# Kernel tuning notes

Measured on AMD Instinct MI355X. Metric: run time of the kernel, lower is better.

## Reference

```python
import jax, jax.numpy as jnp
import numpy as np
from jax import lax
from math import sqrt

STYLE_DIM = 512
K = 3


def _equal_linear(latent, w, b):
    # EqualLinear: runtime weight scaling by 1/sqrt(fan_in)
    scale = 1.0 / sqrt(latent.shape[1])
    return latent @ (w.T * scale) + b


def _pixel_norm(x, axis=1, eps=1e-8):
    return x * jax.lax.rsqrt(jnp.mean(x * x, axis=axis, keepdims=True) + eps)


def _modconv(x, latent, weight, bias, el_w, el_b):
    # weight: (nc2, nc1, 3, 3); x: (B, nc1, H, W); latent: (B, style_dim)
    b = x.shape[0]
    nc2, nc1, k, _ = weight.shape
    fan_in = nc1 * k * k
    w = weight * sqrt(2.0 / fan_in)                      # (nc2, nc1, 3, 3)
    # style: s = 1 + PixelNorm(EqualLinear(latent))      # (B, nc1)
    s = 1.0 + _pixel_norm(_equal_linear(latent, el_w, el_b), axis=1)
    # demod: d_bo = rsqrt(sum_{c,k} (s_bc * w_ock)^2 + 1e-5)
    wsq = jnp.sum(w * w, axis=(2, 3))                    # (nc2, nc1)
    d = jax.lax.rsqrt(jnp.einsum('bc,oc->bo', s * s, wsq) + 1e-5)  # (B, nc2)
    # conv(x, s*w)*d  ==  conv(s*x, w)*d  (s is per input channel)
    xm = x * s[:, :, None, None]
    y = lax.conv_general_dilated(
        xm, w, window_strides=(1, 1), padding=[(1, 1), (1, 1)],
        dimension_numbers=('NCHW', 'OIHW', 'NCHW'))
    return y * d[:, :, None, None] + bias


def _style_block(x, latent, w0, b0, el0_w, el0_b, w1, b1, el1_w, el1_b):
    act_gain = sqrt(2.0)
    out = _modconv(x, latent, w0, b0, el0_w, el0_b)
    out = jax.nn.leaky_relu(out, 0.2) * act_gain
    out = _pixel_norm(out, axis=1)
    out = _modconv(out, latent, w1, b1, el1_w, el1_b)
    out = jax.nn.leaky_relu(out, 0.2) * act_gain
    out = _pixel_norm(out, axis=1)
    return out


def setup_inputs() -> dict:
    key = jax.random.key(0)
    ks = jax.random.split(key, 8)
    B, NC1, NC2, H, W = 8, 256, 256, 128, 128
    return {
        'x': jax.random.normal(ks[0], (B, NC1, H, W), jnp.float32),
        'latent': jax.random.normal(ks[1], (B, STYLE_DIM), jnp.float32),
        'w0': jax.random.normal(ks[2], (NC2, NC1, K, K), jnp.float32),
        'b0': jnp.zeros((1, NC2, 1, 1), jnp.float32),
        'el0_w': jax.random.normal(ks[3], (NC1, STYLE_DIM), jnp.float32),
        'el0_b': jnp.zeros((NC1,), jnp.float32),
        'w1': jax.random.normal(ks[4], (NC2, NC2, K, K), jnp.float32),
        'b1': jnp.zeros((1, NC2, 1, 1), jnp.float32),
        'el1_w': jax.random.normal(ks[5], (NC2, STYLE_DIM), jnp.float32),
        'el1_b': jnp.zeros((NC2,), jnp.float32),
    }


def reference(x, latent, w0, b0, el0_w, el0_b, w1, b1, el1_w, el1_b):
    return _style_block(x, latent, w0, b0, el0_w, el0_b, w1, b1, el1_w, el1_b)
```

## Files before the change

kernel.cpp:

```cpp
#include <hip/hip_runtime.h>
#include <hip/hip_bf16.h>

typedef __attribute__((ext_vector_type(8))) short short8;
typedef __attribute__((ext_vector_type(16))) float f32x16;

typedef const __attribute__((address_space(1))) unsigned int* gas1_t;
typedef __attribute__((address_space(3))) unsigned int* las3_t;

__device__ __forceinline__ unsigned short f2bf(float x) {
    unsigned int u = __float_as_uint(x);
    u = (u + 0x7fffu + ((u >> 16) & 1u)) >> 16;
    return (unsigned short)u;
}

__device__ __forceinline__ int4 pack8(const unsigned short* u) {
    int4 p;
    p.x = (int)((unsigned)u[0] | ((unsigned)u[1] << 16));
    p.y = (int)((unsigned)u[2] | ((unsigned)u[3] << 16));
    p.z = (int)((unsigned)u[4] | ((unsigned)u[5] << 16));
    p.w = (int)((unsigned)u[6] | ((unsigned)u[7] << 16));
    return p;
}

__device__ __forceinline__ void gld_lds16(const void* g, void* l) {
    __builtin_amdgcn_global_load_lds((gas1_t)g, (las3_t)l, 16, 0, 0);
}

__global__ void style_kernel(const float* __restrict__ latent,
                             const float* __restrict__ elw0, const float* __restrict__ elb0,
                             const float* __restrict__ elw1, const float* __restrict__ elb1,
                             float* __restrict__ s_arr) {
    const int cv = blockIdx.x >> 3;
    const int b  = blockIdx.x & 7;
    const int c  = threadIdx.x;
    const float* elw = cv ? elw1 : elw0;
    const float* elb = cv ? elb1 : elb0;

    __shared__ float lat[512];
    lat[c] = latent[b * 512 + c];
    lat[c + 256] = latent[b * 512 + c + 256];
    __syncthreads();

    float accv = 0.f;
    const float* wrow = elw + (size_t)c * 512;
#pragma unroll 8
    for (int k = 0; k < 512; ++k) accv += lat[k] * wrow[k];
    const float lin = accv * 0.04419417382415922f + elb[c];

    float sq = lin * lin;
#pragma unroll
    for (int off = 32; off >= 1; off >>= 1) sq += __shfl_xor(sq, off);
    __shared__ float wsum[4];
    if ((threadIdx.x & 63) == 0) wsum[threadIdx.x >> 6] = sq;
    __syncthreads();
    const float total = wsum[0] + wsum[1] + wsum[2] + wsum[3];
    const float s = 1.0f + lin * rsqrtf(total * (1.0f / 256.0f) + 1e-8f);
    s_arr[(cv * 8 + b) * 256 + c] = s;
}

__global__ void wsq_kernel(const float* __restrict__ w0, const float* __restrict__ w1,
                           float* __restrict__ wsq) {
    const int cv = blockIdx.x >> 8;
    const int o  = blockIdx.x & 255;
    const int c  = threadIdx.x;
    const float* w = cv ? w1 : w0;
    const size_t base = ((size_t)o * 256 + c) * 9;
    float ssum = 0.f;
#pragma unroll
    for (int t = 0; t < 9; ++t) { float v = w[base + t]; ssum += v * v; }
    wsq[((size_t)cv * 256 + o) * 256 + c] = ssum * (2.0f / 2304.0f);
}

__global__ void demod_kernel(const float* __restrict__ s_arr, const float* __restrict__ wsq,
                             float* __restrict__ d_arr) {
    const int cv = blockIdx.x >> 3;
    const int b  = blockIdx.x & 7;
    const int o  = threadIdx.x;
    __shared__ float ss[256];
    float sv = s_arr[(cv * 8 + b) * 256 + o];
    ss[o] = sv * sv;
    __syncthreads();
    const float* wrow = wsq + ((size_t)cv * 256 + o) * 256;
    float accv = 0.f;
#pragma unroll 8
    for (int c = 0; c < 256; ++c) accv += ss[c] * wrow[c];
    d_arr[(cv * 8 + b) * 256 + o] = rsqrtf(accv + 1e-5f);
}

__global__ void fold_kernel(const float* __restrict__ w0, const float* __restrict__ w1,
                            const float* __restrict__ s_arr, const float* __restrict__ d_arr,
                            unsigned short* __restrict__ wm0, unsigned short* __restrict__ wm1) {
    const int cv = blockIdx.y;
    const int e  = blockIdx.x * 256 + threadIdx.x;
    const float* w = cv ? w1 : w0;
    unsigned short* wm = cv ? wm1 : wm0;
    const int slab = e >> 13;
    const int idx  = e & 8191;
    const int b  = slab / 72;
    const int s2 = slab - b * 72;
    const int cc = s2 / 9;
    const int t  = s2 - cc * 9;
    const int o  = idx >> 5;
    const int c5 = idx & 31;
    const int c  = cc * 32 + c5;
    const float val = w[((size_t)o * 256 + c) * 9 + t] * 0.029462782549439483f
                    * s_arr[(cv * 8 + b) * 256 + c] * d_arr[(cv * 8 + b) * 256 + o];
    wm[((size_t)slab << 13) + (c5 >> 3) * 2048 + o * 8 + (c5 & 7)] = f2bf(val);
}

__global__ void convert_kernel(const float* __restrict__ x, unsigned short* __restrict__ xq) {
    const int blk = blockIdx.x;
    const int hh  = blk & 127;
    const int bg_ = blk >> 7;
    const int g   = bg_ & 31;
    const int b   = bg_ >> 5;
    __shared__ float sx[8][128];
    const int tid = threadIdx.x;
#pragma unroll
    for (int i = 0; i < 4; ++i) {
        const int idx = tid + i * 256;
        const int c8 = idx >> 7, p = idx & 127;
        sx[c8][p] = x[(((size_t)b * 256 + g * 8 + c8) * 128 + hh) * 128 + p];
    }
    __syncthreads();
    if (tid < 128) {
        const int p = tid;
        unsigned short u[8];
#pragma unroll
        for (int j = 0; j < 8; ++j) u[j] = f2bf(sx[j][p]);
        *(int4*)(xq + ((((size_t)b * 32 + g) * 128 + hh) * 128 + p) * 8) = pack8(u);
    }
}

template<bool FINAL_OUT>
__global__ __launch_bounds__(512, 2) void conv_kernel(
    const unsigned short* __restrict__ in_q, const unsigned short* __restrict__ wmod,
    const float* __restrict__ bias, const unsigned short* __restrict__ zpg,
    void* __restrict__ out_v) {

    __shared__ __align__(16) char lds[87104];

    const int tid  = threadIdx.x;
    const int b    = blockIdx.x & 7;
    const int rp   = blockIdx.x >> 3;
    const int h0   = rp * 2;
    const int lane = tid & 63;
    const int wr   = tid >> 6;
    const int wm   = wr & 3;
    const int wn   = wr >> 2;
    const int l31  = lane & 31;
    const int khg  = lane >> 5;

    float* sbias = (float*)(lds + 81984);
    if (tid < 256) sbias[tid] = bias[tid];
    if (tid < 4)   *(int4*)(lds + 81920 + tid * 16) = (int4){0, 0, 0, 0};

    int aoff[2][2];
#pragma unroll
    for (int mb = 0; mb < 2; ++mb)
#pragma unroll
        for (int kh = 0; kh < 2; ++kh)
            aoff[mb][kh] = ((khg + 2 * kh) * 256 + wm * 64 + mb * 32 + l31) * 16;

    const unsigned short* wmb = wmod + (size_t)b * 589824;
    const unsigned short* xqb = in_q + (size_t)b * 4194304;

    auto issueA = [&](const char* src, int buf) {
        char* db = lds + buf * 16384 + wr * 2048;
        const char* s = src + wr * 2048 + lane * 16;
        gld_lds16(s,        db);
        gld_lds16(s + 1024, db + 1024);
    };

    auto issueB = [&](int cc) {
        const int chunk = tid >> 7, px = tid & 127;
#pragma unroll
        for (int r = 0; r < 4; ++r) {
            const int hin = h0 - 1 + r;
            const unsigned short* src = ((unsigned)hin < 128u)
                ? xqb + (((size_t)(cc * 4 + chunk) * 128 + hin) * 128 + px) * 8
                : zpg;
            gld_lds16(src, lds + 49152 + r * 8192 + wr * 1024);
        }
    };

    f32x16 acc[2][4];
#pragma unroll
    for (int mb = 0; mb < 2; ++mb)
#pragma unroll
        for (int nb = 0; nb < 4; ++nb)
#pragma unroll
            for (int r = 0; r < 16; ++r) acc[mb][nb][r] = 0.f;

    issueB(0);
    issueA((const char*)wmb, 0);
    issueA((const char*)wmb + 16384, 1);
    __syncthreads();

    const char* gA = (const char*)wmb + 32768;
#pragma unroll 1
    for (int cc = 0; cc < 8; ++cc) {
#pragma unroll
        for (int t = 0; t < 9; ++t) {
            const int dy = t / 3, dx = t - (t / 3) * 3;
            const int cur = t % 3, tgt = (t + 2) % 3;
            const bool doIssue = (t <= 6) || (cc < 7);
            if (doIssue) { issueA(gA, tgt); gA += 16384; }

            const char* Ac = lds + cur * 16384;
            short8 af[2][2], bf[4][2];
#pragma unroll
            for (int mb = 0; mb < 2; ++mb)
#pragma unroll
                for (int kh = 0; kh < 2; ++kh)
                    af[mb][kh] = *(const short8*)(Ac + aoff[mb][kh]);
#pragma unroll
            for (int nb = 0; nb < 4; ++nb)
#pragma unroll
                for (int kh = 0; kh < 2; ++kh) {
                    int off = 49152 + (wn + dy) * 8192 + (khg + 2 * kh) * 2048
                            + (nb * 32 + l31 + dx - 1) * 16;
                    if (dx == 0 && nb == 0) off = (l31 == 0)  ? 81920 : off;
                    if (dx == 2 && nb == 3) off = (l31 == 31) ? 81920 : off;
                    bf[nb][kh] = *(const short8*)(lds + off);
                }

            __builtin_amdgcn_s_setprio(1);
#pragma unroll
            for (int kh = 0; kh < 2; ++kh)
#pragma unroll
                for (int mb = 0; mb < 2; ++mb)
#pragma unroll
                    for (int nb = 0; nb < 4; ++nb)
                        acc[mb][nb] = __builtin_amdgcn_mfma_f32_32x32x16_bf16(
                            af[mb][kh], bf[nb][kh], acc[mb][nb], 0, 0, 0);
            __builtin_amdgcn_s_setprio(0);

            if (doIssue) asm volatile("s_waitcnt vmcnt(2) lgkmcnt(0)" ::: "memory");
            else         asm volatile("s_waitcnt vmcnt(0) lgkmcnt(0)" ::: "memory");
            __builtin_amdgcn_sched_barrier(0);
            __builtin_amdgcn_s_barrier();
        }
        if (cc < 7) {
            issueB(cc + 1);
            asm volatile("s_waitcnt vmcnt(0)" ::: "memory");
            __builtin_amdgcn_sched_barrier(0);
            __builtin_amdgcn_s_barrier();
        }
    }

    float psum[4] = {0.f, 0.f, 0.f, 0.f};
    const float actGain = 1.4142135623730951f;
#pragma unroll
    for (int mb = 0; mb < 2; ++mb)
#pragma unroll
        for (int rg = 0; rg < 16; ++rg) {
            const int row = (rg & 3) + 8 * (rg >> 2) + 4 * khg;
            const float bo = sbias[wm * 64 + mb * 32 + row];
#pragma unroll
            for (int nb = 0; nb < 4; ++nb) {
                float v = acc[mb][nb][rg] + bo;
                v = (v > 0.f ? v : 0.2f * v) * actGain;
                acc[mb][nb][rg] = v;
                psum[nb] += v * v;
            }
        }
#pragma unroll
    for (int nb = 0; nb < 4; ++nb) psum[nb] += __shfl_xor(psum[nb], 32);
    float* red = (float*)(lds + 83008);
    if (lane < 32) {
#pragma unroll
        for (int nb = 0; nb < 4; ++nb)
            red[(wn * 4 + wm) * 128 + nb * 32 + l31] = psum[nb];
    }
    __syncthreads();
    float rs[4];
#pragma unroll
    for (int nb = 0; nb < 4; ++nb) {
        const int p = nb * 32 + l31;
        const float ssum = red[(wn * 4 + 0) * 128 + p] + red[(wn * 4 + 1) * 128 + p]
                         + red[(wn * 4 + 2) * 128 + p] + red[(wn * 4 + 3) * 128 + p];
        rs[nb] = rsqrtf(ssum * (1.0f / 256.0f) + 1e-8f);
    }

    const int h = h0 + wn;
    if (FINAL_OUT) {
        float* outF = (float*)out_v;
#pragma unroll
        for (int mb = 0; mb < 2; ++mb)
#pragma unroll
            for (int rg = 0; rg < 16; ++rg) {
                const int row = (rg & 3) + 8 * (rg >> 2) + 4 * khg;
                const int o = wm * 64 + mb * 32 + row;
                const size_t rb = (((size_t)b * 256 + o) * 128 + h) * 128;
#pragma unroll
                for (int nb = 0; nb < 4; ++nb)
                    outF[rb + nb * 32 + l31] = acc[mb][nb][rg] * rs[nb];
            }
    } else {
        unsigned short* outB = (unsigned short*)out_v;
        char* wreg = lds + wr * 8192;
#pragma unroll
        for (int mb = 0; mb < 2; ++mb) {
#pragma unroll
            for (int rg = 0; rg < 16; rg += 2) {
                const int row = (rg & 3) + 8 * (rg >> 2) + 4 * khg;
#pragma unroll
                for (int nb = 0; nb < 4; ++nb) {
                    const int pxl = nb * 32 + l31;
                    const unsigned lo = f2bf(acc[mb][nb][rg]     * rs[nb]);
                    const unsigned hi = f2bf(acc[mb][nb][rg + 1] * rs[nb]);
                    *(unsigned int*)(wreg + pxl * 64 + (((row >> 3) ^ (pxl & 3)) << 4)
                                     + (row & 7) * 2) = lo | (hi << 16);
                }
            }
            asm volatile("s_waitcnt lgkmcnt(0)" ::: "memory");
#pragma unroll
            for (int oc = 0; oc < 4; ++oc)
#pragma unroll
                for (int ph = 0; ph < 2; ++ph) {
                    const int pxl = ph * 64 + lane;
                    const int4 v = *(const int4*)(wreg + pxl * 64 + ((oc ^ (pxl & 3)) << 4));
                    const int g = wm * 8 + mb * 4 + oc;
                    *(int4*)(outB + ((((size_t)b * 32 + g) * 128 + h) * 128 + pxl) * 8) = v;
                }
            asm volatile("s_waitcnt lgkmcnt(0)" ::: "memory");
        }
    }
}

extern "C" void kernel_launch(void* const* d_in, const int* in_sizes, int n_in,
                              void* d_out, int out_size, void* d_ws, size_t ws_size,
                              hipStream_t stream) {
    (void)in_sizes; (void)n_in; (void)out_size; (void)ws_size;
    const float* x      = (const float*)d_in[0];
    const float* latent = (const float*)d_in[1];
    const float* w0     = (const float*)d_in[2];
    const float* b0     = (const float*)d_in[3];
    const float* el0w   = (const float*)d_in[4];
    const float* el0b   = (const float*)d_in[5];
    const float* w1     = (const float*)d_in[6];
    const float* b1     = (const float*)d_in[7];
    const float* el1w   = (const float*)d_in[8];
    const float* el1b   = (const float*)d_in[9];

    char* ws = (char*)d_ws;
    float* s_arr = (float*)ws;
    float* d_arr = (float*)(ws + 16384);
    float* wsq   = (float*)(ws + 32768);
    unsigned short* zpg = (unsigned short*)(ws + 32768);
    unsigned short* wm0 = (unsigned short*)(ws + 557056);
    unsigned short* wm1 = (unsigned short*)(ws + 9994240);
    unsigned short* xq  = (unsigned short*)(ws + 19431424);
    unsigned short* tmp = (unsigned short*)(ws + 86540288);

    style_kernel<<<16, 256, 0, stream>>>(latent, el0w, el0b, el1w, el1b, s_arr);
    wsq_kernel<<<512, 256, 0, stream>>>(w0, w1, wsq);
    demod_kernel<<<16, 256, 0, stream>>>(s_arr, wsq, d_arr);
    hipMemsetAsync(zpg, 0, 256, stream);
    fold_kernel<<<dim3(18432, 2), 256, 0, stream>>>(w0, w1, s_arr, d_arr, wm0, wm1);
    convert_kernel<<<32768, 256, 0, stream>>>(x, xq);

    conv_kernel<false><<<512, 512, 0, stream>>>(xq, wm0, b0, zpg, tmp);
    conv_kernel<true><<<512, 512, 0, stream>>>(tmp, wm1, b1, zpg, d_out);
}
```

Before: 367.3 us.

## Double-buffer weight tiles in three-tap groups to cut barriers per channel chunk

The weight prefetch changes from a three-slot ring of single 3x3 taps to double-buffered groups of three taps, one kernel row each. Each group is loaded with one larger async global-to-LDS transfer, so there is one wait and barrier per three taps instead of one per tap. LDS use grows to about 136 KB for the two 48 KB weight buffers. The input-row staging is recomputed with an equivalent address formula and stays serialized at each channel-chunk boundary.

```diff
diff --git a/kernel.cpp b/kernel.cpp
--- a/kernel.cpp
+++ b/kernel.cpp
@@ -138,7 +138,7 @@
     const float* __restrict__ bias, const unsigned short* __restrict__ zpg,
     void* __restrict__ out_v) {
 
-    __shared__ __align__(16) char lds[87104];
+    __shared__ __align__(16) char lds[136256];
 
     const int tid  = threadIdx.x;
     const int b    = blockIdx.x & 7;
@@ -151,9 +151,9 @@
     const int l31  = lane & 31;
     const int khg  = lane >> 5;
 
-    float* sbias = (float*)(lds + 81984);
+    float* sbias = (float*)(lds + 131136);
     if (tid < 256) sbias[tid] = bias[tid];
-    if (tid < 4)   *(int4*)(lds + 81920 + tid * 16) = (int4){0, 0, 0, 0};
+    if (tid < 4)   *(int4*)(lds + 131072 + tid * 16) = (int4){0, 0, 0, 0};
 
     int aoff[2][2];
 #pragma unroll
@@ -165,22 +165,26 @@
     const unsigned short* wmb = wmod + (size_t)b * 589824;
     const unsigned short* xqb = in_q + (size_t)b * 4194304;
 
-    auto issueA = [&](const char* src, int buf) {
-        char* db = lds + buf * 16384 + wr * 2048;
+    auto issueA3 = [&](const char* src, int nbuf) {
+        char* db = lds + nbuf * 49152 + wr * 2048;
         const char* s = src + wr * 2048 + lane * 16;
-        gld_lds16(s,        db);
-        gld_lds16(s + 1024, db + 1024);
+#pragma unroll
+        for (int j = 0; j < 3; ++j) {
+            gld_lds16(s + j * 16384,        db + j * 16384);
+            gld_lds16(s + j * 16384 + 1024, db + j * 16384 + 1024);
+        }
     };
 
     auto issueB = [&](int cc) {
-        const int chunk = tid >> 7, px = tid & 127;
+        const int koct = tid >> 7;
+        const int px   = tid & 127;
 #pragma unroll
         for (int r = 0; r < 4; ++r) {
             const int hin = h0 - 1 + r;
             const unsigned short* src = ((unsigned)hin < 128u)
-                ? xqb + (((size_t)(cc * 4 + chunk) * 128 + hin) * 128 + px) * 8
+                ? xqb + (((size_t)(cc * 4 + koct) * 128 + hin) * 128 + px) * 8
                 : zpg;
-            gld_lds16(src, lds + 49152 + r * 8192 + wr * 1024);
+            gld_lds16(src, lds + 98304 + r * 8192 + koct * 2048 + (wr & 1) * 1024);
         }
     };
 
@@ -192,58 +196,54 @@
 #pragma unroll
             for (int r = 0; r < 16; ++r) acc[mb][nb][r] = 0.f;
 
+    issueA3((const char*)wmb, 0);
     issueB(0);
-    issueA((const char*)wmb, 0);
-    issueA((const char*)wmb + 16384, 1);
-    __syncthreads();
-
-    const char* gA = (const char*)wmb + 32768;
+    __syncthreads();
+
+    const char* gA = (const char*)wmb + 49152;
 #pragma unroll 1
     for (int cc = 0; cc < 8; ++cc) {
-#pragma unroll
-        for (int t = 0; t < 9; ++t) {
-            const int dy = t / 3, dx = t - (t / 3) * 3;
-            const int cur = t % 3, tgt = (t + 2) % 3;
-            const bool doIssue = (t <= 6) || (cc < 7);
-            if (doIssue) { issueA(gA, tgt); gA += 16384; }
-
-            const char* Ac = lds + cur * 16384;
-            short8 af[2][2], bf[4][2];
-#pragma unroll
-            for (int mb = 0; mb < 2; ++mb)
-#pragma unroll
-                for (int kh = 0; kh < 2; ++kh)
-                    af[mb][kh] = *(const short8*)(Ac + aoff[mb][kh]);
-#pragma unroll
-            for (int nb = 0; nb < 4; ++nb)
-#pragma unroll
-                for (int kh = 0; kh < 2; ++kh) {
-                    int off = 49152 + (wn + dy) * 8192 + (khg + 2 * kh) * 2048
-                            + (nb * 32 + l31 + dx - 1) * 16;
-                    if (dx == 0 && nb == 0) off = (l31 == 0)  ? 81920 : off;
-                    if (dx == 2 && nb == 3) off = (l31 == 31) ? 81920 : off;
-                    bf[nb][kh] = *(const short8*)(lds + off);
-                }
-
-            __builtin_amdgcn_s_setprio(1);
-#pragma unroll
-            for (int kh = 0; kh < 2; ++kh)
-#pragma unroll
-                for (int mb = 0; mb < 2; ++mb)
-#pragma unroll
-                    for (int nb = 0; nb < 4; ++nb)
-                        acc[mb][nb] = __builtin_amdgcn_mfma_f32_32x32x16_bf16(
-                            af[mb][kh], bf[nb][kh], acc[mb][nb], 0, 0, 0);
-            __builtin_amdgcn_s_setprio(0);
-
-            if (doIssue) asm volatile("s_waitcnt vmcnt(2) lgkmcnt(0)" ::: "memory");
-            else         asm volatile("s_waitcnt vmcnt(0) lgkmcnt(0)" ::: "memory");
+        if (cc > 0) {
+            issueB(cc);
+            asm volatile("s_waitcnt vmcnt(0)" ::: "memory");
             __builtin_amdgcn_sched_barrier(0);
             __builtin_amdgcn_s_barrier();
         }
-        if (cc < 7) {
-            issueB(cc + 1);
-            asm volatile("s_waitcnt vmcnt(0)" ::: "memory");
+#pragma unroll
+        for (int r = 0; r < 3; ++r) {
+            const int g = cc * 3 + r;
+            if (g < 23) { issueA3(gA, (g + 1) & 1); gA += 49152; }
+            const char* Ac = lds + (g & 1) * 49152;
+#pragma unroll
+            for (int i = 0; i < 3; ++i) {
+                short8 af[2][2], bf[4][2];
+#pragma unroll
+                for (int mb = 0; mb < 2; ++mb)
+#pragma unroll
+                    for (int kh = 0; kh < 2; ++kh)
+                        af[mb][kh] = *(const short8*)(Ac + i * 16384 + aoff[mb][kh]);
+#pragma unroll
+                for (int nb = 0; nb < 4; ++nb)
+#pragma unroll
+                    for (int kh = 0; kh < 2; ++kh) {
+                        int off = 98304 + (wn + r) * 8192 + (khg + 2 * kh) * 2048
+                                + (nb * 32 + l31 + i - 1) * 16;
+                        if (i == 0 && nb == 0) off = (l31 == 0)  ? 131072 : off;
+                        if (i == 2 && nb == 3) off = (l31 == 31) ? 131072 : off;
+                        bf[nb][kh] = *(const short8*)(lds + off);
+                    }
+                __builtin_amdgcn_s_setprio(1);
+#pragma unroll
+                for (int kh = 0; kh < 2; ++kh)
+#pragma unroll
+                    for (int mb = 0; mb < 2; ++mb)
+#pragma unroll
+                        for (int nb = 0; nb < 4; ++nb)
+                            acc[mb][nb] = __builtin_amdgcn_mfma_f32_32x32x16_bf16(
+                                af[mb][kh], bf[nb][kh], acc[mb][nb], 0, 0, 0);
+                __builtin_amdgcn_s_setprio(0);
+            }
+            asm volatile("s_waitcnt vmcnt(0) lgkmcnt(0)" ::: "memory");
             __builtin_amdgcn_sched_barrier(0);
             __builtin_amdgcn_s_barrier();
         }
@@ -267,7 +267,7 @@
         }
 #pragma unroll
     for (int nb = 0; nb < 4; ++nb) psum[nb] += __shfl_xor(psum[nb], 32);
-    float* red = (float*)(lds + 83008);
+    float* red = (float*)(lds + 132160);
     if (lane < 32) {
 #pragma unroll
         for (int nb = 0; nb < 4; ++nb)
```

New measurement: 369.4 us. No clear change (+0.6%).
